# Kernel optimization log

Hardware: AMD Instinct MI355X
Metric: run time of the kernel (lower is better)

The kernel has to match this reference:

```python
import jax, jax.numpy as jnp
import numpy as np
import math

B, S, HID = 2, 2048, 4096
NH, NKV, HD = 32, 8, 128
ROPE_BASE = 10000.0


def _rope_tables(b, s, hd):
    inv_freq = 1.0 / (ROPE_BASE ** (jnp.arange(0, hd, 2, dtype=jnp.float32) / hd))
    t = jnp.arange(s, dtype=jnp.float32)
    freqs = jnp.outer(t, inv_freq)            # [s, hd/2]
    emb = jnp.concatenate([freqs, freqs], -1)  # [s, hd]
    cos = jnp.broadcast_to(jnp.cos(emb)[None], (b, s, hd))
    sin = jnp.broadcast_to(jnp.sin(emb)[None], (b, s, hd))
    return cos, sin


def setup_inputs() -> dict:
    key = jax.random.key(0)
    ks = jax.random.split(key, 5)
    hidden_states = jax.random.normal(ks[0], (B, S, HID), dtype=jnp.float32)
    # additive causal mask [B,1,S,S]: 0 on/below diagonal, large negative above
    causal = jnp.tril(jnp.ones((S, S), dtype=bool))
    attention_mask = jnp.where(causal, 0.0, jnp.finfo(jnp.float32).min)[None, None]
    attention_mask = jnp.broadcast_to(attention_mask, (B, 1, S, S)).astype(jnp.float32)
    cos, sin = _rope_tables(B, S, HD)
    sc = 0.02
    Wq = jax.random.normal(ks[1], (NH * HD, HID), dtype=jnp.float32) * sc
    Wk = jax.random.normal(ks[2], (NKV * HD, HID), dtype=jnp.float32) * sc
    Wv = jax.random.normal(ks[3], (NKV * HD, HID), dtype=jnp.float32) * sc
    Wo = jax.random.normal(ks[4], (HID, NH * HD), dtype=jnp.float32) * sc
    return {"hidden_states": hidden_states, "attention_mask": attention_mask,
            "cos": cos, "sin": sin, "Wq": Wq, "Wk": Wk, "Wv": Wv, "Wo": Wo}


def _rotate_half(x):
    x1, x2 = jnp.split(x, 2, axis=-1)
    return jnp.concatenate([-x2, x1], axis=-1)


def reference(hidden_states, attention_mask, cos, sin, Wq, Wk, Wv, Wo):
    b, s, _ = hidden_states.shape
    # projections (nn.Linear: x @ W.T, no bias)
    q = jnp.einsum('bsh,oh->bso', hidden_states, Wq).reshape(b, s, NH, HD).transpose(0, 2, 1, 3)
    k = jnp.einsum('bsh,oh->bso', hidden_states, Wk).reshape(b, s, NKV, HD).transpose(0, 2, 1, 3)
    v = jnp.einsum('bsh,oh->bso', hidden_states, Wv).reshape(b, s, NKV, HD).transpose(0, 2, 1, 3)
    # RoPE (cos/sin: [b,s,hd] -> unsqueeze head dim)
    c, sn = cos[:, None], sin[:, None]
    q = q * c + _rotate_half(q) * sn
    k = k * c + _rotate_half(k) * sn
    # repeat_kv: [b,nkv,s,d] -> [b,nh,s,d] (repeat_interleave over head dim)
    n_rep = NH // NKV
    k = jnp.repeat(k, n_rep, axis=1)
    v = jnp.repeat(v, n_rep, axis=1)
    # eager attention
    scores = jnp.einsum('bhqd,bhkd->bhqk', q, k) / math.sqrt(HD)
    scores = scores + attention_mask[:, :, :, :k.shape[2]]
    probs = jax.nn.softmax(scores.astype(jnp.float32), axis=-1).astype(q.dtype)
    attn = jnp.einsum('bhqk,bhkd->bhqd', probs, v)
    attn = attn.transpose(0, 2, 1, 3).reshape(b, s, NH * HD)
    return jnp.einsum('bso,ho->bsh', attn, Wo)
```

## Files before the change

kernel.cpp:

```cpp
#include <hip/hip_runtime.h>
#include <hip/hip_bf16.h>
#include <cstdint>

#define S_LEN 2048
#define HIDDEN 4096
#define NH 32
#define NKV 8
#define HD 128
#define BATCH 2
#define MROWS (BATCH * S_LEN)

typedef float f32x4 __attribute__((ext_vector_type(4)));
typedef __bf16 bf16x8 __attribute__((ext_vector_type(8)));
typedef __bf16 bf16x4 __attribute__((ext_vector_type(4)));

static __device__ inline f32x4 mfma16(bf16x8 a, bf16x8 b, f32x4 c) {
    return __builtin_amdgcn_mfma_f32_16x16x32_bf16(a, b, c, 0, 0, 0);
}

static __device__ inline void gl_lds16(const __bf16* g, __bf16* l) {
    __builtin_amdgcn_global_load_lds(
        (const __attribute__((address_space(1))) void*)g,
        (__attribute__((address_space(3))) void*)l, 16, 0, 0);
}

#define LGKM0()  asm volatile("s_waitcnt lgkmcnt(0)" ::: "memory")
#define SCHEDB() __builtin_amdgcn_sched_barrier(0)
#define SBAR()   __builtin_amdgcn_s_barrier()

static __device__ inline void conv8(const float* src, __bf16* dst, int i) {
    const float4* p = (const float4*)src + (size_t)i * 2;
    float4 a = p[0], b = p[1];
    bf16x8 v;
    v[0] = (__bf16)a.x; v[1] = (__bf16)a.y; v[2] = (__bf16)a.z; v[3] = (__bf16)a.w;
    v[4] = (__bf16)b.x; v[5] = (__bf16)b.y; v[6] = (__bf16)b.z; v[7] = (__bf16)b.w;
    ((bf16x8*)dst)[i] = v;
}

__global__ __launch_bounds__(256) void conv_f32_bf16(const float* __restrict__ in,
                                                     __bf16* __restrict__ out, int n8) {
    int i = blockIdx.x * 256 + threadIdx.x;
    if (i >= n8) return;
    conv8(in, out, i);
}

__global__ __launch_bounds__(256) void conv4(const float* __restrict__ s0, __bf16* __restrict__ d0, int b0,
                                             const float* __restrict__ s1, __bf16* __restrict__ d1, int b1,
                                             const float* __restrict__ s2, __bf16* __restrict__ d2, int b2,
                                             const float* __restrict__ s3, __bf16* __restrict__ d3) {
    int blk = blockIdx.x;
    const float* s; __bf16* d; int base;
    if (blk < b0)                { s = s0; d = d0; base = blk; }
    else if (blk < b0 + b1)      { s = s1; d = d1; base = blk - b0; }
    else if (blk < b0 + b1 + b2) { s = s2; d = d2; base = blk - b0 - b1; }
    else                         { s = s3; d = d3; base = blk - b0 - b1 - b2; }
    conv8(s, d, base * 256 + threadIdx.x);
}

template<int MODE, int BM>
__global__ __launch_bounds__(512, 2) void gemm256(const __bf16* __restrict__ A,
                                                  const __bf16* __restrict__ B,
                                                  float* __restrict__ Cf,
                                                  __bf16* __restrict__ Qo,
                                                  __bf16* __restrict__ Ko,
                                                  __bf16* __restrict__ Vo,
                                                  int N, int K, int nbx) {
    constexpr int MF = BM / 32;
    constexpr int MH = BM / 64;
    __shared__ __bf16 As[2][BM * 64];
    __shared__ __bf16 Bs[2][256 * 64];
    const int tid = threadIdx.x, lane = tid & 63;
    const int lq = lane & 15, hi2 = lane >> 4;
    const int wv = tid >> 6;
    const int wr = wv >> 2, wc = wv & 3;

    const int cpx = gridDim.x >> 3;
    const int bid = blockIdx.x;
    const int swz = (bid & 7) * cpx + (bid >> 3);
    const int bx = swz % nbx, by = swz / nbx;
    const int brow = by * BM, bcol = bx * 256;

    f32x4 acc[MF][4] = {};
    bf16x8 af[MH][2], bfr[2][2];
    const int NT = K >> 6;

    auto stageA = [&](int bb, int kt, int roff) {
        #pragma unroll
        for (int r = 0; r < 2; ++r) {
            int i = r * 512 + tid;
            int row = i >> 3, sl = i & 7, lsl = sl ^ (row & 7);
            gl_lds16(A + (size_t)(brow + roff + row) * K + kt * 64 + lsl * 8,
                     &As[bb][roff * 64 + i * 8]);
        }
    };
    auto stageB = [&](int bb, int kt, int roff) {
        #pragma unroll
        for (int r = 0; r < 2; ++r) {
            int i = r * 512 + tid;
            int row = i >> 3, sl = i & 7, lsl = sl ^ (row & 7);
            gl_lds16(B + (size_t)(bcol + roff + row) * K + kt * 64 + lsl * 8,
                     &Bs[bb][roff * 64 + i * 8]);
        }
    };
    auto loadA = [&](int bb, int mq) {
        #pragma unroll
        for (int mi = 0; mi < MH; ++mi) {
            int row = wr * (BM / 2) + (mq * MH + mi) * 16 + lq;
            #pragma unroll
            for (int kk = 0; kk < 2; ++kk) {
                int lsl = (kk * 4 + hi2) ^ (row & 7);
                af[mi][kk] = *(const bf16x8*)&As[bb][row * 64 + lsl * 8];
            }
        }
    };
    auto loadB = [&](int bb, int nq) {
        #pragma unroll
        for (int ni = 0; ni < 2; ++ni) {
            int row = wc * 64 + (nq * 2 + ni) * 16 + lq;
            #pragma unroll
            for (int kk = 0; kk < 2; ++kk) {
                int lsl = (kk * 4 + hi2) ^ (row & 7);
                bfr[ni][kk] = *(const bf16x8*)&Bs[bb][row * 64 + lsl * 8];
            }
        }
    };
    auto mmaq = [&](int mq, int nq) {
        __builtin_amdgcn_s_setprio(1);
        #pragma unroll
        for (int kk = 0; kk < 2; ++kk)
            #pragma unroll
            for (int mi = 0; mi < MH; ++mi)
                #pragma unroll
                for (int ni = 0; ni < 2; ++ni)
                    acc[mq * MH + mi][nq * 2 + ni] =
                        mfma16(af[mi][kk], bfr[ni][kk], acc[mq * MH + mi][nq * 2 + ni]);
        __builtin_amdgcn_s_setprio(0);
    };

    stageA(0, 0, 0);
    if constexpr (BM == 256) stageA(0, 0, 128);
    stageB(0, 0, 0);
    stageB(0, 0, 128);

    for (int t = 0; t < NT; ++t) {
        const int cur = t & 1, nxt = cur ^ 1;
        const int tn = (t + 1 < NT) ? t + 1 : NT - 1;
        stageA(nxt, tn, 0);
        if constexpr (BM == 256) stageA(nxt, tn, 128);
        stageB(nxt, tn, 0);
        if constexpr (BM == 256) { asm volatile("s_waitcnt vmcnt(6)" ::: "memory"); }
        else                     { asm volatile("s_waitcnt vmcnt(4)" ::: "memory"); }
        SBAR(); SCHEDB();
        loadA(cur, 0); loadB(cur, 0);
        LGKM0(); SCHEDB();
        mmaq(0, 0);
        SBAR(); SCHEDB();
        loadB(cur, 1);
        stageB(nxt, tn, 128);
        SBAR(); SCHEDB();
        LGKM0(); SCHEDB();
        mmaq(0, 1);
        SBAR(); SCHEDB();
        loadA(cur, 1);
        SBAR(); SCHEDB();
        LGKM0(); SCHEDB();
        mmaq(1, 1);
        SBAR(); SCHEDB();
        loadB(cur, 0);
        SBAR(); SCHEDB();
        LGKM0(); SCHEDB();
        mmaq(1, 0);
        SBAR(); SCHEDB();
    }

    #pragma unroll
    for (int m = 0; m < MF; ++m) {
        #pragma unroll
        for (int n = 0; n < 4; ++n) {
            int row0 = brow + wr * (BM / 2) + m * 16 + (hi2 << 2);
            int col  = bcol + wc * 64 + n * 16 + lq;
            if constexpr (MODE == 3) {
                if (col < NKV * HD) {
                    #pragma unroll
                    for (int j = 0; j < 4; ++j)
                        Ko[(size_t)(row0 + j) * (NKV * HD) + col] = (__bf16)acc[m][n][j];
                } else {
                    int c2 = col - NKV * HD;
                    int hkv = c2 >> 7, d = c2 & (HD - 1);
                    int bb2 = row0 >> 11, s = row0 & (S_LEN - 1);
                    bf16x4 t4;
                    #pragma unroll
                    for (int j = 0; j < 4; ++j) t4[j] = (__bf16)acc[m][n][j];
                    *(bf16x4*)&Vo[((size_t)((bb2 * NKV + hkv) * HD + d)) * S_LEN + s] = t4;
                }
            } else if constexpr (MODE == 1) {
                #pragma unroll
                for (int j = 0; j < 4; ++j)
                    Cf[(size_t)(row0 + j) * N + col] = acc[m][n][j];
            } else {
                #pragma unroll
                for (int j = 0; j < 4; ++j)
                    Qo[(size_t)(row0 + j) * N + col] = (__bf16)acc[m][n][j];
            }
        }
    }
}

__global__ __launch_bounds__(256) void rope_kernel(__bf16* __restrict__ X,
                                                   const float* __restrict__ ct,
                                                   const float* __restrict__ st,
                                                   int nheads, int total) {
    int idx = blockIdx.x * 256 + threadIdx.x;
    if (idx >= total) return;
    int d  = idx & 63;
    int hh = (idx >> 6) % nheads;
    int m  = idx / (64 * nheads);
    __bf16* p = X + (size_t)m * (nheads * HD) + hh * HD;
    float c = ct[(size_t)m * HD + d];
    float s = st[(size_t)m * HD + d];
    float x1 = (float)p[d], x2 = (float)p[d + 64];
    p[d]      = (__bf16)(x1 * c - x2 * s);
    p[d + 64] = (__bf16)(x2 * c + x1 * s);
}

__global__ __launch_bounds__(256, 3) void attn_kernel(const __bf16* __restrict__ Q,
                                                      const __bf16* __restrict__ K,
                                                      const __bf16* __restrict__ V,
                                                      __bf16* __restrict__ O,
                                                      const float* __restrict__ ct,
                                                      const float* __restrict__ st) {
    constexpr int QB = 128, KB = 32;
    constexpr int nqb = S_LEN / QB;
    const int cpx = gridDim.x >> 3;
    const int b0 = blockIdx.x;
    const int bid = (b0 & 7) * cpx + (b0 >> 3);
    const int pair = bid & 7;
    const int h    = (bid >> 3) & (NH - 1);
    const int b    = bid >> 8;
    const int hkv = h >> 2;
    const int tid = threadIdx.x, lane = tid & 63, w = tid >> 6;
    const int lq = lane & 15, hi2 = lane >> 4;

    __shared__ __bf16 Ks[2][KB * HD];
    __shared__ __bf16 Vt[2][HD * KB];
    __shared__ __bf16 Pl[4][2][16][40];

    const int qbA = nqb - 1 - pair;
    const int nkbA = 4 * (qbA + 1);
    const int T = nkbA + 4 * (pair + 1);

    auto stage = [&](int bb, int k0s) {
        #pragma unroll
        for (int r = 0; r < 2; ++r) {
            int i = r * 256 + tid;
            {   int row = i >> 4, sl = i & 15, lsl = sl ^ (row & 7);
                gl_lds16(&K[((size_t)(b * S_LEN + k0s + row)) * (NKV * HD) + hkv * HD + lsl * 8],
                         &Ks[bb][i * 8]); }
            {   int d = i >> 2, sl = i & 3, lsl = sl ^ (d & 3);
                gl_lds16(&V[((size_t)((b * NKV + hkv) * HD + d)) * S_LEN + k0s + lsl * 8],
                         &Vt[bb][i * 8]); }
        }
    };

    const float c2 = 0.08838834764831843f * 1.4426950408889634f;

    stage(0, 0);
    int tt = 0;
    #pragma unroll 1
    for (int pass = 0; pass < 2; ++pass) {
        const int qb = pass ? pair : qbA;
        const int q0 = qb * QB, qrow_lo = q0 + w * 32;
        const int nkb = 4 * (qb + 1);

        bf16x8 qf[2][4];
        #pragma unroll
        for (int mt = 0; mt < 2; ++mt) {
            int row = qrow_lo + mt * 16 + lq;
            const __bf16* qp = Q + ((size_t)(b * S_LEN + row)) * (NH * HD) + h * HD + hi2 * 8;
            const float* cp = ct + ((size_t)(b * S_LEN + row)) * HD + hi2 * 8;
            const float* sp = st + ((size_t)(b * S_LEN + row)) * HD + hi2 * 8;
            #pragma unroll
            for (int c = 0; c < 2; ++c) {
                bf16x8 lo = *(const bf16x8*)(qp + c * 32);
                bf16x8 hi = *(const bf16x8*)(qp + c * 32 + 64);
                f32x4 c0 = *(const f32x4*)(cp + c * 32);
                f32x4 c1 = *(const f32x4*)(cp + c * 32 + 4);
                f32x4 s0 = *(const f32x4*)(sp + c * 32);
                f32x4 s1 = *(const f32x4*)(sp + c * 32 + 4);
                bf16x8 rlo, rhi;
                #pragma unroll
                for (int e = 0; e < 8; ++e) {
                    float cc = ((e < 4) ? c0[e] : c1[e - 4]) * c2;
                    float ss = ((e < 4) ? s0[e] : s1[e - 4]) * c2;
                    float xl = (float)lo[e], xh = (float)hi[e];
                    rlo[e] = (__bf16)(xl * cc - xh * ss);
                    rhi[e] = (__bf16)(xh * cc + xl * ss);
                }
                qf[mt][c]     = rlo;
                qf[mt][c + 2] = rhi;
            }
        }

        f32x4 o_acc[2][8] = {};
        float m_r[2] = {-1e30f, -1e30f}, l_r[2] = {0.f, 0.f};

        #pragma unroll 1
        for (int kb = 0; kb < nkb; ++kb, ++tt) {
            int tn = (tt + 1 < T) ? tt + 1 : T - 1;
            int k0n = (tn < nkbA ? tn : tn - nkbA) * KB;
            stage((tt + 1) & 1, k0n);
            asm volatile("s_waitcnt vmcnt(4)" ::: "memory");
            SBAR(); SCHEDB();
            const int cur = tt & 1;
            const int k0  = kb * KB;
            const __bf16* ks = &Ks[cur][0];
            const __bf16* vt = &Vt[cur][0];

            f32x4 sc[2][2] = {};
            #pragma unroll
            for (int t = 0; t < 2; ++t) {
                int krow = t * 16 + lq;
                #pragma unroll
                for (int c = 0; c < 4; ++c) {
                    int psl = (c * 4 + hi2) ^ (krow & 7);
                    bf16x8 kf = *(const bf16x8*)&ks[krow * HD + psl * 8];
                    sc[0][t] = mfma16(kf, qf[0][c], sc[0][t]);
                    sc[1][t] = mfma16(kf, qf[1][c], sc[1][t]);
                }
            }

            #pragma unroll
            for (int mt = 0; mt < 2; ++mt) {
                int q_abs = qrow_lo + mt * 16 + lq;
                if (k0 + KB - 1 > qrow_lo + mt * 16) {
                    #pragma unroll
                    for (int t = 0; t < 2; ++t)
                        #pragma unroll
                        for (int j = 0; j < 4; ++j) {
                            int kv_abs = k0 + t * 16 + hi2 * 4 + j;
                            if (kv_abs > q_abs) sc[mt][t][j] = -1e30f;
                        }
                }
                float pmax = fmaxf(
                    fmaxf(fmaxf(sc[mt][0][0], sc[mt][0][1]), fmaxf(sc[mt][0][2], sc[mt][0][3])),
                    fmaxf(fmaxf(sc[mt][1][0], sc[mt][1][1]), fmaxf(sc[mt][1][2], sc[mt][1][3])));
                pmax = fmaxf(pmax, __shfl_xor(pmax, 16));
                pmax = fmaxf(pmax, __shfl_xor(pmax, 32));
                if (!__all(pmax - m_r[mt] <= 8.0f)) {
                    float mn = fmaxf(m_r[mt], pmax);
                    float sf = __builtin_amdgcn_exp2f(m_r[mt] - mn);
                    m_r[mt] = mn;
                    l_r[mt] *= sf;
                    #pragma unroll
                    for (int dt = 0; dt < 8; ++dt)
                        #pragma unroll
                        for (int j = 0; j < 4; ++j) o_acc[mt][dt][j] *= sf;
                }
                float rs = 0.f;
                #pragma unroll
                for (int t = 0; t < 2; ++t)
                    #pragma unroll
                    for (int j = 0; j < 4; ++j) {
                        float p = __builtin_amdgcn_exp2f(sc[mt][t][j] - m_r[mt]);
                        sc[mt][t][j] = p;
                        rs += p;
                    }
                rs += __shfl_xor(rs, 16);
                rs += __shfl_xor(rs, 32);
                l_r[mt] += rs;
                #pragma unroll
                for (int t = 0; t < 2; ++t) {
                    bf16x4 pw;
                    #pragma unroll
                    for (int j = 0; j < 4; ++j) pw[j] = (__bf16)sc[mt][t][j];
                    *(bf16x4*)&Pl[w][mt][lq][t * 16 + hi2 * 4] = pw;
                }
            }

            LGKM0(); SCHEDB();
            bf16x8 pf0 = *(const bf16x8*)&Pl[w][0][lq][hi2 * 8];
            bf16x8 pf1 = *(const bf16x8*)&Pl[w][1][lq][hi2 * 8];

            #pragma unroll
            for (int dt = 0; dt < 8; ++dt) {
                int vrow = dt * 16 + lq;
                int psl  = hi2 ^ (vrow & 3);
                bf16x8 vf = *(const bf16x8*)&vt[vrow * KB + psl * 8];
                o_acc[0][dt] = mfma16(vf, pf0, o_acc[0][dt]);
                o_acc[1][dt] = mfma16(vf, pf1, o_acc[1][dt]);
            }
            LGKM0(); SCHEDB();
            SBAR(); SCHEDB();
        }

        #pragma unroll
        for (int mt = 0; mt < 2; ++mt) {
            float inv = 1.0f / l_r[mt];
            int q_abs = qrow_lo + mt * 16 + lq;
            __bf16* op = O + ((size_t)(b * S_LEN + q_abs)) * (NH * HD) + h * HD;
            #pragma unroll
            for (int dt = 0; dt < 8; ++dt) {
                bf16x4 t4;
                #pragma unroll
                for (int j = 0; j < 4; ++j) t4[j] = (__bf16)(o_acc[mt][dt][j] * inv);
                *(bf16x4*)&op[dt * 16 + hi2 * 4] = t4;
            }
        }
    }
}

extern "C" void kernel_launch(void* const* d_in, const int* in_sizes, int n_in,
                              void* d_out, int out_size, void* d_ws, size_t ws_size,
                              hipStream_t stream) {
    const float* X  = (const float*)d_in[0];
    const float* ct = (const float*)d_in[2];
    const float* st = (const float*)d_in[3];
    const float* Wq = (const float*)d_in[4];
    const float* Wk = (const float*)d_in[5];
    const float* Wv = (const float*)d_in[6];
    const float* Wo = (const float*)d_in[7];
    float* out = (float*)d_out;

    const size_t MEL  = (size_t)MROWS * HIDDEN;
    const size_t KVEL = (size_t)MROWS * (NKV * HD);
    const int NQKV = NH * HD + 2 * NKV * HD;

    __bf16* Wqkv = (__bf16*)d_ws;
    __bf16* Xb   = Wqkv + (size_t)NQKV * HIDDEN;
    __bf16* Qb   = Xb + MEL;
    __bf16* Kb   = Qb + MEL;
    __bf16* VtG  = Kb + KVEL;
    __bf16* Ab   = Wqkv;
    __bf16* Wob  = Xb;

    dim3 blk(256);
    const int cbM = (int)(MEL / 8 / 256);
    const int cbK = (int)(KVEL / 8 / 256);
    hipLaunchKernelGGL(conv4, dim3(2 * cbM + 2 * cbK), blk, 0, stream,
                       X,  Xb, cbM,
                       Wq, Wqkv, cbM,
                       Wk, Wqkv + (size_t)HIDDEN * HIDDEN, cbK,
                       Wv, Wqkv + (size_t)(HIDDEN + NKV * HD) * HIDDEN);

    hipLaunchKernelGGL((gemm256<0, 256>), dim3(256), dim3(512), 0, stream,
                       Xb, Wqkv, nullptr, Qb, nullptr, nullptr, NH * HD, HIDDEN, 16);
    hipLaunchKernelGGL((gemm256<3, 128>), dim3(256), dim3(512), 0, stream,
                       Xb, Wqkv + (size_t)HIDDEN * HIDDEN, nullptr, nullptr, Kb, VtG,
                       2 * NKV * HD, HIDDEN, 8);

    hipLaunchKernelGGL(rope_kernel, dim3((MROWS * NKV * 64) / 256), blk, 0, stream,
                       Kb, ct, st, NKV, MROWS * NKV * 64);

    hipLaunchKernelGGL(conv_f32_bf16, dim3(cbM), blk, 0, stream, Wo, Wob, (int)(MEL / 8));

    hipLaunchKernelGGL(attn_kernel, dim3(512), blk, 0, stream, Qb, Kb, VtG, Ab, ct, st);

    hipLaunchKernelGGL((gemm256<1, 256>), dim3(256), dim3(512), 0, stream,
                       Ab, Wob, out, nullptr, nullptr, nullptr, HIDDEN, HIDDEN, 16);
}
```

Before: 559.7 us.

## Split paired causal q-blocks into separate workgroups with higher occupancy and MFMA priority

Replaces the paired-q-block scheme, where each workgroup processed a long and a short causal q-block back to back, with one q-block per workgroup and twice the grid, scheduling the longest blocks first. The launch bound rises to 4 waves per SIMD, the P staging buffer shrinks to one tile per wave (reused across the two m-tiles), and s_setprio raises wave priority around the MFMA sections. This adds parallelism and occupancy but gives up the implicit load balancing of pairing and may cause tail imbalance or register pressure.

```diff
diff --git a/kernel.cpp b/kernel.cpp
--- a/kernel.cpp
+++ b/kernel.cpp
@@ -223,7 +223,7 @@
     p[d + 64] = (__bf16)(x2 * c + x1 * s);
 }
 
-__global__ __launch_bounds__(256, 3) void attn_kernel(const __bf16* __restrict__ Q,
+__global__ __launch_bounds__(256, 4) void attn_kernel(const __bf16* __restrict__ Q,
                                                       const __bf16* __restrict__ K,
                                                       const __bf16* __restrict__ V,
                                                       __bf16* __restrict__ O,
@@ -234,20 +234,19 @@
     const int cpx = gridDim.x >> 3;
     const int b0 = blockIdx.x;
     const int bid = (b0 & 7) * cpx + (b0 >> 3);
-    const int pair = bid & 7;
-    const int h    = (bid >> 3) & (NH - 1);
-    const int b    = bid >> 8;
+    const int qb  = nqb - 1 - (bid % nqb);
+    const int h   = (bid / nqb) % NH;
+    const int b   = bid / (nqb * NH);
     const int hkv = h >> 2;
     const int tid = threadIdx.x, lane = tid & 63, w = tid >> 6;
     const int lq = lane & 15, hi2 = lane >> 4;
+    const int q0 = qb * QB, qrow_lo = q0 + w * 32;
 
     __shared__ __bf16 Ks[2][KB * HD];
     __shared__ __bf16 Vt[2][HD * KB];
-    __shared__ __bf16 Pl[4][2][16][40];
-
-    const int qbA = nqb - 1 - pair;
-    const int nkbA = 4 * (qbA + 1);
-    const int T = nkbA + 4 * (pair + 1);
+    __shared__ __bf16 Pl[4][16][40];
+
+    const int nkb = 4 * (qb + 1);
 
     auto stage = [&](int bb, int k0s) {
         #pragma unroll
@@ -264,147 +263,141 @@
 
     const float c2 = 0.08838834764831843f * 1.4426950408889634f;
 
+    bf16x8 qf[2][4];
+    #pragma unroll
+    for (int mt = 0; mt < 2; ++mt) {
+        int row = qrow_lo + mt * 16 + lq;
+        const __bf16* qp = Q + ((size_t)(b * S_LEN + row)) * (NH * HD) + h * HD + hi2 * 8;
+        const float* cp = ct + ((size_t)(b * S_LEN + row)) * HD + hi2 * 8;
+        const float* sp = st + ((size_t)(b * S_LEN + row)) * HD + hi2 * 8;
+        #pragma unroll
+        for (int c = 0; c < 2; ++c) {
+            bf16x8 lo = *(const bf16x8*)(qp + c * 32);
+            bf16x8 hi = *(const bf16x8*)(qp + c * 32 + 64);
+            f32x4 c0 = *(const f32x4*)(cp + c * 32);
+            f32x4 c1 = *(const f32x4*)(cp + c * 32 + 4);
+            f32x4 s0 = *(const f32x4*)(sp + c * 32);
+            f32x4 s1 = *(const f32x4*)(sp + c * 32 + 4);
+            bf16x8 rlo, rhi;
+            #pragma unroll
+            for (int e = 0; e < 8; ++e) {
+                float cc = ((e < 4) ? c0[e] : c1[e - 4]) * c2;
+                float ss = ((e < 4) ? s0[e] : s1[e - 4]) * c2;
+                float xl = (float)lo[e], xh = (float)hi[e];
+                rlo[e] = (__bf16)(xl * cc - xh * ss);
+                rhi[e] = (__bf16)(xh * cc + xl * ss);
+            }
+            qf[mt][c]     = rlo;
+            qf[mt][c + 2] = rhi;
+        }
+    }
+
+    f32x4 o_acc[2][8] = {};
+    float m_r[2] = {-1e30f, -1e30f}, l_r[2] = {0.f, 0.f};
+
     stage(0, 0);
-    int tt = 0;
     #pragma unroll 1
-    for (int pass = 0; pass < 2; ++pass) {
-        const int qb = pass ? pair : qbA;
-        const int q0 = qb * QB, qrow_lo = q0 + w * 32;
-        const int nkb = 4 * (qb + 1);
-
-        bf16x8 qf[2][4];
+    for (int kb = 0; kb < nkb; ++kb) {
+        int kn = (kb + 1 < nkb) ? kb + 1 : kb;
+        stage((kb + 1) & 1, kn * KB);
+        asm volatile("s_waitcnt vmcnt(4)" ::: "memory");
+        SBAR(); SCHEDB();
+        const int cur = kb & 1;
+        const int k0  = kb * KB;
+        const __bf16* ks = &Ks[cur][0];
+        const __bf16* vt = &Vt[cur][0];
+
+        f32x4 sc[2][2] = {};
+        __builtin_amdgcn_s_setprio(1);
+        #pragma unroll
+        for (int t = 0; t < 2; ++t) {
+            int krow = t * 16 + lq;
+            #pragma unroll
+            for (int c = 0; c < 4; ++c) {
+                int psl = (c * 4 + hi2) ^ (krow & 7);
+                bf16x8 kf = *(const bf16x8*)&ks[krow * HD + psl * 8];
+                sc[0][t] = mfma16(kf, qf[0][c], sc[0][t]);
+                sc[1][t] = mfma16(kf, qf[1][c], sc[1][t]);
+            }
+        }
+        __builtin_amdgcn_s_setprio(0);
+
+        bf16x8 pf[2];
         #pragma unroll
         for (int mt = 0; mt < 2; ++mt) {
-            int row = qrow_lo + mt * 16 + lq;
-            const __bf16* qp = Q + ((size_t)(b * S_LEN + row)) * (NH * HD) + h * HD + hi2 * 8;
-            const float* cp = ct + ((size_t)(b * S_LEN + row)) * HD + hi2 * 8;
-            const float* sp = st + ((size_t)(b * S_LEN + row)) * HD + hi2 * 8;
-            #pragma unroll
-            for (int c = 0; c < 2; ++c) {
-                bf16x8 lo = *(const bf16x8*)(qp + c * 32);
-                bf16x8 hi = *(const bf16x8*)(qp + c * 32 + 64);
-                f32x4 c0 = *(const f32x4*)(cp + c * 32);
-                f32x4 c1 = *(const f32x4*)(cp + c * 32 + 4);
-                f32x4 s0 = *(const f32x4*)(sp + c * 32);
-                f32x4 s1 = *(const f32x4*)(sp + c * 32 + 4);
-                bf16x8 rlo, rhi;
-                #pragma unroll
-                for (int e = 0; e < 8; ++e) {
-                    float cc = ((e < 4) ? c0[e] : c1[e - 4]) * c2;
-                    float ss = ((e < 4) ? s0[e] : s1[e - 4]) * c2;
-                    float xl = (float)lo[e], xh = (float)hi[e];
-                    rlo[e] = (__bf16)(xl * cc - xh * ss);
-                    rhi[e] = (__bf16)(xh * cc + xl * ss);
-                }
-                qf[mt][c]     = rlo;
-                qf[mt][c + 2] = rhi;
-            }
-        }
-
-        f32x4 o_acc[2][8] = {};
-        float m_r[2] = {-1e30f, -1e30f}, l_r[2] = {0.f, 0.f};
-
-        #pragma unroll 1
-        for (int kb = 0; kb < nkb; ++kb, ++tt) {
-            int tn = (tt + 1 < T) ? tt + 1 : T - 1;
-            int k0n = (tn < nkbA ? tn : tn - nkbA) * KB;
-            stage((tt + 1) & 1, k0n);
-            asm volatile("s_waitcnt vmcnt(4)" ::: "memory");
-            SBAR(); SCHEDB();
-            const int cur = tt & 1;
-            const int k0  = kb * KB;
-            const __bf16* ks = &Ks[cur][0];
-            const __bf16* vt = &Vt[cur][0];
-
-            f32x4 sc[2][2] = {};
-            #pragma unroll
-            for (int t = 0; t < 2; ++t) {
-                int krow = t * 16 + lq;
-                #pragma unroll
-                for (int c = 0; c < 4; ++c) {
-                    int psl = (c * 4 + hi2) ^ (krow & 7);
-                    bf16x8 kf = *(const bf16x8*)&ks[krow * HD + psl * 8];
-                    sc[0][t] = mfma16(kf, qf[0][c], sc[0][t]);
-                    sc[1][t] = mfma16(kf, qf[1][c], sc[1][t]);
-                }
-            }
-
-            #pragma unroll
-            for (int mt = 0; mt < 2; ++mt) {
-                int q_abs = qrow_lo + mt * 16 + lq;
-                if (k0 + KB - 1 > qrow_lo + mt * 16) {
-                    #pragma unroll
-                    for (int t = 0; t < 2; ++t)
-                        #pragma unroll
-                        for (int j = 0; j < 4; ++j) {
-                            int kv_abs = k0 + t * 16 + hi2 * 4 + j;
-                            if (kv_abs > q_abs) sc[mt][t][j] = -1e30f;
-                        }
-                }
-                float pmax = fmaxf(
-                    fmaxf(fmaxf(sc[mt][0][0], sc[mt][0][1]), fmaxf(sc[mt][0][2], sc[mt][0][3])),
-                    fmaxf(fmaxf(sc[mt][1][0], sc[mt][1][1]), fmaxf(sc[mt][1][2], sc[mt][1][3])));
-                pmax = fmaxf(pmax, __shfl_xor(pmax, 16));
-                pmax = fmaxf(pmax, __shfl_xor(pmax, 32));
-                if (!__all(pmax - m_r[mt] <= 8.0f)) {
-                    float mn = fmaxf(m_r[mt], pmax);
-                    float sf = __builtin_amdgcn_exp2f(m_r[mt] - mn);
-                    m_r[mt] = mn;
-                    l_r[mt] *= sf;
-                    #pragma unroll
-                    for (int dt = 0; dt < 8; ++dt)
-                        #pragma unroll
-                        for (int j = 0; j < 4; ++j) o_acc[mt][dt][j] *= sf;
-                }
-                float rs = 0.f;
+            int q_abs = qrow_lo + mt * 16 + lq;
+            if (k0 + KB - 1 > qrow_lo + mt * 16) {
                 #pragma unroll
                 for (int t = 0; t < 2; ++t)
                     #pragma unroll
                     for (int j = 0; j < 4; ++j) {
-                        float p = __builtin_amdgcn_exp2f(sc[mt][t][j] - m_r[mt]);
-                        sc[mt][t][j] = p;
-                        rs += p;
+                        int kv_abs = k0 + t * 16 + hi2 * 4 + j;
+                        if (kv_abs > q_abs) sc[mt][t][j] = -1e30f;
                     }
-                rs += __shfl_xor(rs, 16);
-                rs += __shfl_xor(rs, 32);
-                l_r[mt] += rs;
-                #pragma unroll
-                for (int t = 0; t < 2; ++t) {
-                    bf16x4 pw;
+            }
+            float pmax = fmaxf(
+                fmaxf(fmaxf(sc[mt][0][0], sc[mt][0][1]), fmaxf(sc[mt][0][2], sc[mt][0][3])),
+                fmaxf(fmaxf(sc[mt][1][0], sc[mt][1][1]), fmaxf(sc[mt][1][2], sc[mt][1][3])));
+            pmax = fmaxf(pmax, __shfl_xor(pmax, 16));
+            pmax = fmaxf(pmax, __shfl_xor(pmax, 32));
+            if (!__all(pmax - m_r[mt] <= 8.0f)) {
+                float mn = fmaxf(m_r[mt], pmax);
+                float sf = __builtin_amdgcn_exp2f(m_r[mt] - mn);
+                m_r[mt] = mn;
+                l_r[mt] *= sf;
+                #pragma unroll
+                for (int dt = 0; dt < 8; ++dt)
                     #pragma unroll
-                    for (int j = 0; j < 4; ++j) pw[j] = (__bf16)sc[mt][t][j];
-                    *(bf16x4*)&Pl[w][mt][lq][t * 16 + hi2 * 4] = pw;
+                    for (int j = 0; j < 4; ++j) o_acc[mt][dt][j] *= sf;
+            }
+            float rs = 0.f;
+            #pragma unroll
+            for (int t = 0; t < 2; ++t)
+                #pragma unroll
+                for (int j = 0; j < 4; ++j) {
+                    float p = __builtin_amdgcn_exp2f(sc[mt][t][j] - m_r[mt]);
+                    sc[mt][t][j] = p;
+                    rs += p;
                 }
-            }
-
+            rs += __shfl_xor(rs, 16);
+            rs += __shfl_xor(rs, 32);
+            l_r[mt] += rs;
+            #pragma unroll
+            for (int t = 0; t < 2; ++t) {
+                bf16x4 pw;
+                #pragma unroll
+                for (int j = 0; j < 4; ++j) pw[j] = (__bf16)sc[mt][t][j];
+                *(bf16x4*)&Pl[w][lq][t * 16 + hi2 * 4] = pw;
+            }
             LGKM0(); SCHEDB();
-            bf16x8 pf0 = *(const bf16x8*)&Pl[w][0][lq][hi2 * 8];
-            bf16x8 pf1 = *(const bf16x8*)&Pl[w][1][lq][hi2 * 8];
-
-            #pragma unroll
-            for (int dt = 0; dt < 8; ++dt) {
-                int vrow = dt * 16 + lq;
-                int psl  = hi2 ^ (vrow & 3);
-                bf16x8 vf = *(const bf16x8*)&vt[vrow * KB + psl * 8];
-                o_acc[0][dt] = mfma16(vf, pf0, o_acc[0][dt]);
-                o_acc[1][dt] = mfma16(vf, pf1, o_acc[1][dt]);
-            }
-            LGKM0(); SCHEDB();
-            SBAR(); SCHEDB();
-        }
-
-        #pragma unroll
-        for (int mt = 0; mt < 2; ++mt) {
-            float inv = 1.0f / l_r[mt];
-            int q_abs = qrow_lo + mt * 16 + lq;
-            __bf16* op = O + ((size_t)(b * S_LEN + q_abs)) * (NH * HD) + h * HD;
-            #pragma unroll
-            for (int dt = 0; dt < 8; ++dt) {
-                bf16x4 t4;
-                #pragma unroll
-                for (int j = 0; j < 4; ++j) t4[j] = (__bf16)(o_acc[mt][dt][j] * inv);
-                *(bf16x4*)&op[dt * 16 + hi2 * 4] = t4;
-            }
+            pf[mt] = *(const bf16x8*)&Pl[w][lq][hi2 * 8];
+        }
+
+        __builtin_amdgcn_s_setprio(1);
+        #pragma unroll
+        for (int dt = 0; dt < 8; ++dt) {
+            int vrow = dt * 16 + lq;
+            int psl  = hi2 ^ (vrow & 3);
+            bf16x8 vf = *(const bf16x8*)&vt[vrow * KB + psl * 8];
+            o_acc[0][dt] = mfma16(vf, pf[0], o_acc[0][dt]);
+            o_acc[1][dt] = mfma16(vf, pf[1], o_acc[1][dt]);
+        }
+        __builtin_amdgcn_s_setprio(0);
+        LGKM0(); SCHEDB();
+        SBAR(); SCHEDB();
+    }
+
+    #pragma unroll
+    for (int mt = 0; mt < 2; ++mt) {
+        float inv = 1.0f / l_r[mt];
+        int q_abs = qrow_lo + mt * 16 + lq;
+        __bf16* op = O + ((size_t)(b * S_LEN + q_abs)) * (NH * HD) + h * HD;
+        #pragma unroll
+        for (int dt = 0; dt < 8; ++dt) {
+            bf16x4 t4;
+            #pragma unroll
+            for (int j = 0; j < 4; ++j) t4[j] = (__bf16)(o_acc[mt][dt][j] * inv);
+            *(bf16x4*)&op[dt * 16 + hi2 * 4] = t4;
         }
     }
 }
@@ -453,7 +446,7 @@
 
     hipLaunchKernelGGL(conv_f32_bf16, dim3(cbM), blk, 0, stream, Wo, Wob, (int)(MEL / 8));
 
-    hipLaunchKernelGGL(attn_kernel, dim3(512), blk, 0, stream, Qb, Kb, VtG, Ab, ct, st);
+    hipLaunchKernelGGL(attn_kernel, dim3(1024), blk, 0, stream, Qb, Kb, VtG, Ab, ct, st);
 
     hipLaunchKernelGGL((gemm256<1, 256>), dim3(256), dim3(512), 0, stream,
                        Ab, Wob, out, nullptr, nullptr, nullptr, HIDDEN, HIDDEN, 16);
```

Result: slower. 952.5 us (+70.2%).
